# Optimization experiments

Hardware: AMD Instinct MI355X
Metric: run time of the kernel (lower is better)

Reference implementation:

```python
import jax, jax.numpy as jnp
import numpy as np

N = 4            # expansion_rate
C = 1024         # input_dim
STREAM = N * C   # 4096
B, L = 8, 2048
SK_ITERS = 20


def setup_inputs() -> dict:
    key = jax.random.key(0)
    k1, k2 = jax.random.split(key)
    x_flat = jax.random.normal(k1, (B, L, STREAM), dtype=jnp.float32)
    scale = jnp.ones((STREAM,), dtype=jnp.float32)                      # RMSNorm scale
    phi = jax.random.normal(k2, (STREAM, N * N + 2 * N), dtype=jnp.float32) * 0.02
    bias = jnp.zeros((1, N * N + 2 * N), dtype=jnp.float32)
    alpha_pre = jnp.float32(0.01)
    alpha_post = jnp.float32(0.01)
    alpha_res = jnp.float32(0.01)
    return {"x_flat": x_flat, "scale": scale, "phi": phi, "bias": bias,
            "alpha_pre": alpha_pre, "alpha_post": alpha_post, "alpha_res": alpha_res}


def reference(x_flat, scale, phi, bias, alpha_pre, alpha_post, alpha_res):
    n = N
    b, l, _ = x_flat.shape
    # RMSNorm over last dim
    rms = jnp.sqrt(jnp.mean(x_flat * x_flat, axis=-1, keepdims=True) + 1e-20)
    x_norm = scale * x_flat / rms
    # single fused projection -> split into pre / post / res mappings
    m = jnp.einsum('bld,de->ble', x_norm, phi) + bias  # [B,L,n*n+2n]
    h_pre = jax.nn.sigmoid(alpha_pre * m[..., :n])                      # [B,L,n]
    h_post = 2.0 * jax.nn.sigmoid(alpha_post * m[..., n:2 * n])         # [B,L,n]
    h_res = jnp.exp(alpha_res * m[..., 2 * n:].reshape(b, l, n, n))     # [B,L,n,n]
    # Sinkhorn-Knopp: alternating row / column normalization
    def body(_, M):
        M = M / (M.sum(axis=-1, keepdims=True) + 1e-12)
        M = M / (M.sum(axis=-2, keepdims=True) + 1e-12)
        return M
    h_res = jax.lax.fori_loop(0, SK_ITERS, body, h_res)
    return (h_pre, h_post, h_res)
```

## Files before the change

kernel.cpp:

```cpp
#include <hip/hip_runtime.h>
#include <math.h>

#define NEXP 4
#define STREAM 4096
#define NOUT 24
#define NTOK 16384
#define SK_ITERS 20

#define T_PER_BLOCK 8
#define CHUNK 512
#define NCHUNK (STREAM / CHUNK)

__global__ __launch_bounds__(256) void k_transpose_scale(
    const float* __restrict__ phi, const float* __restrict__ scale,
    float* __restrict__ phiT) {
  int flat = blockIdx.x * 256 + threadIdx.x;
  int k = flat / NOUT;
  int j = flat - k * NOUT;
  phiT[j * STREAM + k] = phi[flat] * scale[k];
}

__global__ __launch_bounds__(256) void k_fused(
    const float* __restrict__ x, const float* __restrict__ phiT,
    const float* __restrict__ bias,
    const float* __restrict__ a_pre_p, const float* __restrict__ a_post_p,
    const float* __restrict__ a_res_p, float* __restrict__ out) {
  __shared__ float lds_x[T_PER_BLOCK * CHUNK];
  __shared__ float lds_inv[T_PER_BLOCK];
  __shared__ float lds_m[T_PER_BLOCK * NOUT];

  const int tid  = threadIdx.x;
  const int w    = tid >> 6;
  const int lane = tid & 63;
  const int tok0 = blockIdx.x * T_PER_BLOCK;

  const float4* x4    = (const float4*)x;
  const float4* phiT4 = (const float4*)phiT;
  float4*       lds4  = (float4*)lds_x;

  float acc[T_PER_BLOCK][6];
#pragma unroll
  for (int t = 0; t < T_PER_BLOCK; t++)
#pragma unroll
    for (int jj = 0; jj < 6; jj++) acc[t][jj] = 0.0f;
  float ssq0 = 0.0f, ssq1 = 0.0f;

  for (int ch = 0; ch < NCHUNK; ch++) {
#pragma unroll
    for (int tl = 0; tl < 2; tl++) {
      int t = 2 * w + tl;
      int tok = tok0 + t;
#pragma unroll
      for (int i = 0; i < 2; i++) {
        int pos4 = i * 64 + lane;
        float4 v = x4[tok * (STREAM / 4) + ch * (CHUNK / 4) + pos4];
        lds4[t * (CHUNK / 4) + pos4] = v;
        float s = v.x * v.x + v.y * v.y + v.z * v.z + v.w * v.w;
        if (tl == 0) ssq0 += s; else ssq1 += s;
      }
    }
    __syncthreads();
#pragma unroll
    for (int i = 0; i < 2; i++) {
      int k4 = i * 64 + lane;
      float4 p[6];
#pragma unroll
      for (int jj = 0; jj < 6; jj++)
        p[jj] = phiT4[(6 * w + jj) * (STREAM / 4) + ch * (CHUNK / 4) + k4];
#pragma unroll
      for (int t = 0; t < T_PER_BLOCK; t++) {
        float4 xv = lds4[t * (CHUNK / 4) + k4];
#pragma unroll
        for (int jj = 0; jj < 6; jj++) {
          float a = acc[t][jj];
          a = fmaf(xv.x, p[jj].x, a);
          a = fmaf(xv.y, p[jj].y, a);
          a = fmaf(xv.z, p[jj].z, a);
          a = fmaf(xv.w, p[jj].w, a);
          acc[t][jj] = a;
        }
      }
    }
    __syncthreads();
  }

#pragma unroll
  for (int d = 1; d < 64; d <<= 1) {
    ssq0 += __shfl_xor(ssq0, d, 64);
    ssq1 += __shfl_xor(ssq1, d, 64);
  }
  if (lane == 0) {
    lds_inv[2 * w]     = 1.0f / sqrtf(ssq0 * (1.0f / STREAM) + 1e-20f);
    lds_inv[2 * w + 1] = 1.0f / sqrtf(ssq1 * (1.0f / STREAM) + 1e-20f);
  }

#pragma unroll
  for (int d = 1; d < 64; d <<= 1) {
#pragma unroll
    for (int t = 0; t < T_PER_BLOCK; t++)
#pragma unroll
      for (int jj = 0; jj < 6; jj++)
        acc[t][jj] += __shfl_xor(acc[t][jj], d, 64);
  }
  __syncthreads();

#pragma unroll
  for (int t = 0; t < T_PER_BLOCK; t++) {
    float inv = lds_inv[t];
#pragma unroll
    for (int jj = 0; jj < 6; jj++) {
      if (lane == t * 6 + jj) {
        int j = 6 * w + jj;
        lds_m[t * NOUT + j] = acc[t][jj] * inv + bias[j];
      }
    }
  }
  __syncthreads();

  if (tid < T_PER_BLOCK * 16) {
    int t = tid >> 4;
    int e = tid & 15;
    int tok = tok0 + t;

    float a_res = *a_res_p;
    float M = expf(a_res * lds_m[t * NOUT + 2 * NEXP + e]);
#pragma unroll 1
    for (int it = 0; it < SK_ITERS; it++) {
      float rs = M + __shfl_xor(M, 1, 64);
      rs += __shfl_xor(rs, 2, 64);
      M = M / (rs + 1e-12f);
      float cs = M + __shfl_xor(M, 4, 64);
      cs += __shfl_xor(cs, 8, 64);
      M = M / (cs + 1e-12f);
    }
    out[2 * NTOK * NEXP + tok * 16 + e] = M;

    if (e < NEXP) {
      float z = (*a_pre_p) * lds_m[t * NOUT + e];
      out[tok * NEXP + e] = 1.0f / (1.0f + expf(-z));
    } else if (e < 2 * NEXP) {
      int j = e - NEXP;
      float z = (*a_post_p) * lds_m[t * NOUT + NEXP + j];
      out[NTOK * NEXP + tok * NEXP + j] = 2.0f / (1.0f + expf(-z));
    }
  }
}

extern "C" void kernel_launch(void* const* d_in, const int* in_sizes, int n_in,
                              void* d_out, int out_size, void* d_ws, size_t ws_size,
                              hipStream_t stream) {
  const float* x      = (const float*)d_in[0];
  const float* scale  = (const float*)d_in[1];
  const float* phi    = (const float*)d_in[2];
  const float* bias   = (const float*)d_in[3];
  const float* a_pre  = (const float*)d_in[4];
  const float* a_post = (const float*)d_in[5];
  const float* a_res  = (const float*)d_in[6];
  float* out = (float*)d_out;

  float* phiT = (float*)d_ws;

  k_transpose_scale<<<(NOUT * STREAM) / 256, 256, 0, stream>>>(phi, scale, phiT);
  k_fused<<<NTOK / T_PER_BLOCK, 256, 0, stream>>>(x, phiT, bias, a_pre, a_post,
                                                  a_res, out);
}
```

Before: 409.0 us.

## Double-buffer x chunks in LDS with register prefetch of next chunk

```diff
diff --git a/kernel.cpp b/kernel.cpp
--- a/kernel.cpp
+++ b/kernel.cpp
@@ -20,14 +20,70 @@
   phiT[j * STREAM + k] = phi[flat] * scale[k];
 }
 
+__device__ __forceinline__ void chunk_step(
+    int ch, int w, int lane, int rowA, int rowB,
+    const float4* __restrict__ x4, const float4* __restrict__ phiT4,
+    const float* bufC, float* bufN,
+    float (&acc)[T_PER_BLOCK][6], float& ssq0, float& ssq1) {
+  float4 a0, a1, b0, b1;
+  const bool pref = (ch + 1 < NCHUNK);
+
+  __syncthreads();
+
+  if (pref) {
+    int off = (ch + 1) * (CHUNK / 4);
+    a0 = x4[rowA + off + lane];
+    a1 = x4[rowA + off + 64 + lane];
+    b0 = x4[rowB + off + lane];
+    b1 = x4[rowB + off + 64 + lane];
+  }
+
+  const float4* l4 = (const float4*)bufC;
+  const int pbase = (6 * w) * (STREAM / 4) + ch * (CHUNK / 4);
+#pragma unroll
+  for (int i = 0; i < 2; i++) {
+    int k4 = i * 64 + lane;
+    float4 p[6];
+#pragma unroll
+    for (int jj = 0; jj < 6; jj++)
+      p[jj] = phiT4[pbase + jj * (STREAM / 4) + k4];
+#pragma unroll
+    for (int t = 0; t < T_PER_BLOCK; t++) {
+      float4 xv = l4[t * (CHUNK / 4) + k4];
+#pragma unroll
+      for (int jj = 0; jj < 6; jj++) {
+        float a = acc[t][jj];
+        a = fmaf(xv.x, p[jj].x, a);
+        a = fmaf(xv.y, p[jj].y, a);
+        a = fmaf(xv.z, p[jj].z, a);
+        a = fmaf(xv.w, p[jj].w, a);
+        acc[t][jj] = a;
+      }
+    }
+  }
+
+  if (pref) {
+    float4* n4 = (float4*)bufN;
+    n4[(2 * w) * (CHUNK / 4) + lane]          = a0;
+    n4[(2 * w) * (CHUNK / 4) + 64 + lane]     = a1;
+    n4[(2 * w + 1) * (CHUNK / 4) + lane]      = b0;
+    n4[(2 * w + 1) * (CHUNK / 4) + 64 + lane] = b1;
+    ssq0 += a0.x * a0.x + a0.y * a0.y + a0.z * a0.z + a0.w * a0.w;
+    ssq0 += a1.x * a1.x + a1.y * a1.y + a1.z * a1.z + a1.w * a1.w;
+    ssq1 += b0.x * b0.x + b0.y * b0.y + b0.z * b0.z + b0.w * b0.w;
+    ssq1 += b1.x * b1.x + b1.y * b1.y + b1.z * b1.z + b1.w * b1.w;
+  }
+}
+
 __global__ __launch_bounds__(256) void k_fused(
     const float* __restrict__ x, const float* __restrict__ phiT,
     const float* __restrict__ bias,
     const float* __restrict__ a_pre_p, const float* __restrict__ a_post_p,
     const float* __restrict__ a_res_p, float* __restrict__ out) {
-  __shared__ float lds_x[T_PER_BLOCK * CHUNK];
+  __shared__ float lds_x0[T_PER_BLOCK * CHUNK];
+  __shared__ float lds_x1[T_PER_BLOCK * CHUNK];
+  __shared__ float lds_m[T_PER_BLOCK * NOUT];
   __shared__ float lds_inv[T_PER_BLOCK];
-  __shared__ float lds_m[T_PER_BLOCK * NOUT];
 
   const int tid  = threadIdx.x;
   const int w    = tid >> 6;
@@ -36,7 +92,6 @@
 
   const float4* x4    = (const float4*)x;
   const float4* phiT4 = (const float4*)phiT;
-  float4*       lds4  = (float4*)lds_x;
 
   float acc[T_PER_BLOCK][6];
 #pragma unroll
@@ -45,43 +100,30 @@
     for (int jj = 0; jj < 6; jj++) acc[t][jj] = 0.0f;
   float ssq0 = 0.0f, ssq1 = 0.0f;
 
-  for (int ch = 0; ch < NCHUNK; ch++) {
-#pragma unroll
-    for (int tl = 0; tl < 2; tl++) {
-      int t = 2 * w + tl;
-      int tok = tok0 + t;
-#pragma unroll
-      for (int i = 0; i < 2; i++) {
-        int pos4 = i * 64 + lane;
-        float4 v = x4[tok * (STREAM / 4) + ch * (CHUNK / 4) + pos4];
-        lds4[t * (CHUNK / 4) + pos4] = v;
-        float s = v.x * v.x + v.y * v.y + v.z * v.z + v.w * v.w;
-        if (tl == 0) ssq0 += s; else ssq1 += s;
-      }
-    }
-    __syncthreads();
-#pragma unroll
-    for (int i = 0; i < 2; i++) {
-      int k4 = i * 64 + lane;
-      float4 p[6];
-#pragma unroll
-      for (int jj = 0; jj < 6; jj++)
-        p[jj] = phiT4[(6 * w + jj) * (STREAM / 4) + ch * (CHUNK / 4) + k4];
-#pragma unroll
-      for (int t = 0; t < T_PER_BLOCK; t++) {
-        float4 xv = lds4[t * (CHUNK / 4) + k4];
-#pragma unroll
-        for (int jj = 0; jj < 6; jj++) {
-          float a = acc[t][jj];
-          a = fmaf(xv.x, p[jj].x, a);
-          a = fmaf(xv.y, p[jj].y, a);
-          a = fmaf(xv.z, p[jj].z, a);
-          a = fmaf(xv.w, p[jj].w, a);
-          acc[t][jj] = a;
-        }
-      }
-    }
-    __syncthreads();
+  const int rowA = (tok0 + 2 * w) * (STREAM / 4);
+  const int rowB = rowA + (STREAM / 4);
+
+  {
+    float4 a0 = x4[rowA + lane];
+    float4 a1 = x4[rowA + 64 + lane];
+    float4 b0 = x4[rowB + lane];
+    float4 b1 = x4[rowB + 64 + lane];
+    float4* n4 = (float4*)lds_x0;
+    n4[(2 * w) * (CHUNK / 4) + lane]          = a0;
+    n4[(2 * w) * (CHUNK / 4) + 64 + lane]     = a1;
+    n4[(2 * w + 1) * (CHUNK / 4) + lane]      = b0;
+    n4[(2 * w + 1) * (CHUNK / 4) + 64 + lane] = b1;
+    ssq0 += a0.x * a0.x + a0.y * a0.y + a0.z * a0.z + a0.w * a0.w;
+    ssq0 += a1.x * a1.x + a1.y * a1.y + a1.z * a1.z + a1.w * a1.w;
+    ssq1 += b0.x * b0.x + b0.y * b0.y + b0.z * b0.z + b0.w * b0.w;
+    ssq1 += b1.x * b1.x + b1.y * b1.y + b1.z * b1.z + b1.w * b1.w;
+  }
+
+  for (int ch = 0; ch < NCHUNK; ch += 2) {
+    chunk_step(ch,     w, lane, rowA, rowB, x4, phiT4, lds_x0, lds_x1,
+               acc, ssq0, ssq1);
+    chunk_step(ch + 1, w, lane, rowA, rowB, x4, phiT4, lds_x1, lds_x0,
+               acc, ssq0, ssq1);
   }
 
 #pragma unroll
@@ -122,7 +164,10 @@
     int e = tid & 15;
     int tok = tok0 + t;
 
-    float a_res = *a_res_p;
+    const float a_res  = *a_res_p;
+    const float a_pre  = *a_pre_p;
+    const float a_post = *a_post_p;
+
     float M = expf(a_res * lds_m[t * NOUT + 2 * NEXP + e]);
 #pragma unroll 1
     for (int it = 0; it < SK_ITERS; it++) {
@@ -136,11 +181,11 @@
     out[2 * NTOK * NEXP + tok * 16 + e] = M;
 
     if (e < NEXP) {
-      float z = (*a_pre_p) * lds_m[t * NOUT + e];
+      float z = a_pre * lds_m[t * NOUT + e];
       out[tok * NEXP + e] = 1.0f / (1.0f + expf(-z));
     } else if (e < 2 * NEXP) {
       int j = e - NEXP;
-      float z = (*a_post_p) * lds_m[t * NOUT + NEXP + j];
+      float z = a_post * lds_m[t * NOUT + NEXP + j];
       out[NTOK * NEXP + tok * NEXP + j] = 2.0f / (1.0f + expf(-z));
     }
   }
```

Measured after the change: 465.3 us. +13.8%, slower.

## Double-buffer x chunks in LDS with async global_load_lds prefetch

Applied to the files above, without the earlier changes.

```diff
diff --git a/kernel.cpp b/kernel.cpp
--- a/kernel.cpp
+++ b/kernel.cpp
@@ -20,23 +20,79 @@
   phiT[j * STREAM + k] = phi[flat] * scale[k];
 }
 
-__global__ __launch_bounds__(256) void k_fused(
+typedef const void __attribute__((address_space(1)))* gas_ptr;
+typedef void __attribute__((address_space(3)))* las_ptr;
+__device__ __forceinline__ void gl_lds16(const float* g, float* s) {
+  __builtin_amdgcn_global_load_lds((gas_ptr)g, (las_ptr)s, 16, 0, 0);
+}
+
+__device__ __forceinline__ void stage_issue(
+    int ch, int w, int lane, const float* xA, const float* xB, float* buf) {
+  const float* gA = xA + ch * CHUNK;
+  const float* gB = xB + ch * CHUNK;
+  float* dA = buf + (2 * w) * CHUNK;
+  float* dB = buf + (2 * w + 1) * CHUNK;
+  gl_lds16(gA + 4 * lane,       dA + 4 * lane);
+  gl_lds16(gA + 256 + 4 * lane, dA + 256 + 4 * lane);
+  gl_lds16(gB + 4 * lane,       dB + 4 * lane);
+  gl_lds16(gB + 256 + 4 * lane, dB + 256 + 4 * lane);
+}
+
+__device__ __forceinline__ void compute_chunk(
+    int ch, int w, int lane, const float4* __restrict__ phiT4,
+    const float* bufC, float (&acc)[T_PER_BLOCK][6],
+    float& ssq0, float& ssq1) {
+  const float4* l4 = (const float4*)bufC;
+  const int pbase = (6 * w) * (STREAM / 4) + ch * (CHUNK / 4);
+#pragma unroll
+  for (int i = 0; i < 2; i++) {
+    int k4 = i * 64 + lane;
+    float4 p[6];
+#pragma unroll
+    for (int jj = 0; jj < 6; jj++)
+      p[jj] = phiT4[pbase + jj * (STREAM / 4) + k4];
+    {
+      float4 va = l4[(2 * w) * (CHUNK / 4) + k4];
+      float sa = va.x * va.x + va.y * va.y + va.z * va.z + va.w * va.w;
+      ssq0 += sa;
+      float4 vb = l4[(2 * w + 1) * (CHUNK / 4) + k4];
+      float sb = vb.x * vb.x + vb.y * vb.y + vb.z * vb.z + vb.w * vb.w;
+      ssq1 += sb;
+    }
+#pragma unroll
+    for (int t = 0; t < T_PER_BLOCK; t++) {
+      float4 xv = l4[t * (CHUNK / 4) + k4];
+#pragma unroll
+      for (int jj = 0; jj < 6; jj++) {
+        float a = acc[t][jj];
+        a = fmaf(xv.x, p[jj].x, a);
+        a = fmaf(xv.y, p[jj].y, a);
+        a = fmaf(xv.z, p[jj].z, a);
+        a = fmaf(xv.w, p[jj].w, a);
+        acc[t][jj] = a;
+      }
+    }
+  }
+}
+
+__global__ __launch_bounds__(256, 4) void k_fused(
     const float* __restrict__ x, const float* __restrict__ phiT,
     const float* __restrict__ bias,
     const float* __restrict__ a_pre_p, const float* __restrict__ a_post_p,
     const float* __restrict__ a_res_p, float* __restrict__ out) {
-  __shared__ float lds_x[T_PER_BLOCK * CHUNK];
+  __shared__ float lds_x0[T_PER_BLOCK * CHUNK];
+  __shared__ float lds_x1[T_PER_BLOCK * CHUNK];
+  __shared__ float lds_m[T_PER_BLOCK * NOUT];
   __shared__ float lds_inv[T_PER_BLOCK];
-  __shared__ float lds_m[T_PER_BLOCK * NOUT];
 
   const int tid  = threadIdx.x;
   const int w    = tid >> 6;
   const int lane = tid & 63;
   const int tok0 = blockIdx.x * T_PER_BLOCK;
 
-  const float4* x4    = (const float4*)x;
   const float4* phiT4 = (const float4*)phiT;
-  float4*       lds4  = (float4*)lds_x;
+  const float* xA = x + (size_t)(tok0 + 2 * w) * STREAM;
+  const float* xB = xA + STREAM;
 
   float acc[T_PER_BLOCK][6];
 #pragma unroll
@@ -45,43 +101,15 @@
     for (int jj = 0; jj < 6; jj++) acc[t][jj] = 0.0f;
   float ssq0 = 0.0f, ssq1 = 0.0f;
 
+  stage_issue(0, w, lane, xA, xB, lds_x0);
+
   for (int ch = 0; ch < NCHUNK; ch++) {
-#pragma unroll
-    for (int tl = 0; tl < 2; tl++) {
-      int t = 2 * w + tl;
-      int tok = tok0 + t;
-#pragma unroll
-      for (int i = 0; i < 2; i++) {
-        int pos4 = i * 64 + lane;
-        float4 v = x4[tok * (STREAM / 4) + ch * (CHUNK / 4) + pos4];
-        lds4[t * (CHUNK / 4) + pos4] = v;
-        float s = v.x * v.x + v.y * v.y + v.z * v.z + v.w * v.w;
-        if (tl == 0) ssq0 += s; else ssq1 += s;
-      }
-    }
+    float* bufC = (ch & 1) ? lds_x1 : lds_x0;
+    float* bufN = (ch & 1) ? lds_x0 : lds_x1;
     __syncthreads();
-#pragma unroll
-    for (int i = 0; i < 2; i++) {
-      int k4 = i * 64 + lane;
-      float4 p[6];
-#pragma unroll
-      for (int jj = 0; jj < 6; jj++)
-        p[jj] = phiT4[(6 * w + jj) * (STREAM / 4) + ch * (CHUNK / 4) + k4];
-#pragma unroll
-      for (int t = 0; t < T_PER_BLOCK; t++) {
-        float4 xv = lds4[t * (CHUNK / 4) + k4];
-#pragma unroll
-        for (int jj = 0; jj < 6; jj++) {
-          float a = acc[t][jj];
-          a = fmaf(xv.x, p[jj].x, a);
-          a = fmaf(xv.y, p[jj].y, a);
-          a = fmaf(xv.z, p[jj].z, a);
-          a = fmaf(xv.w, p[jj].w, a);
-          acc[t][jj] = a;
-        }
-      }
-    }
-    __syncthreads();
+    if (ch + 1 < NCHUNK)
+      stage_issue(ch + 1, w, lane, xA, xB, bufN);
+    compute_chunk(ch, w, lane, phiT4, bufC, acc, ssq0, ssq1);
   }
 
 #pragma unroll
@@ -122,7 +150,10 @@
     int e = tid & 15;
     int tok = tok0 + t;
 
-    float a_res = *a_res_p;
+    const float a_res  = *a_res_p;
+    const float a_pre  = *a_pre_p;
+    const float a_post = *a_post_p;
+
     float M = expf(a_res * lds_m[t * NOUT + 2 * NEXP + e]);
 #pragma unroll 1
     for (int it = 0; it < SK_ITERS; it++) {
@@ -136,11 +167,11 @@
     out[2 * NTOK * NEXP + tok * 16 + e] = M;
 
     if (e < NEXP) {
-      float z = (*a_pre_p) * lds_m[t * NOUT + e];
+      float z = a_pre * lds_m[t * NOUT + e];
       out[tok * NEXP + e] = 1.0f / (1.0f + expf(-z));
     } else if (e < 2 * NEXP) {
       int j = e - NEXP;
-      float z = (*a_post_p) * lds_m[t * NOUT + NEXP + j];
+      float z = a_post * lds_m[t * NOUT + NEXP + j];
       out[NTOK * NEXP + tok * NEXP + j] = 2.0f / (1.0f + expf(-z));
     }
   }
```

Result: slower. 601.2 us (+47.0%).
